# Kernel tuning notes

Hardware: AMD Instinct MI355X
Metric: run time of the kernel (lower is better)

## Reference

```python
import jax, jax.numpy as jnp
import numpy as np

HIDDEN = 1024
NUM_HEADS = 16
HEAD_DIM = HIDDEN // NUM_HEADS
SCALE = HEAD_DIM ** -0.5
BATCH = 32
T_CACHED = 2047


def setup_inputs() -> dict:
    key = jax.random.key(0)
    ks = jax.random.split(key, 8)
    hidden_states = jax.random.normal(ks[0], (BATCH, 1, HIDDEN), dtype=jnp.float32)
    key_cache = jax.random.normal(ks[1], (BATCH, NUM_HEADS, T_CACHED, HEAD_DIM), dtype=jnp.float32)
    value_cache = jax.random.normal(ks[2], (BATCH, NUM_HEADS, T_CACHED, HEAD_DIM), dtype=jnp.float32)
    block_tables = jax.random.randint(ks[3], (BATCH, 128), 0, 1024, dtype=jnp.int64 if jax.config.jax_enable_x64 else jnp.int32)
    # valid lengths in [1, T_cached+1]
    seq_lens = jax.random.randint(ks[4], (BATCH,), 1, T_CACHED + 2, dtype=jnp.int32)
    W_attn = jax.random.normal(ks[5], (HIDDEN, 3 * HIDDEN), dtype=jnp.float32) * (HIDDEN ** -0.5)
    b_attn = jnp.zeros((3 * HIDDEN,), dtype=jnp.float32)
    W_proj = jax.random.normal(ks[6], (HIDDEN, HIDDEN), dtype=jnp.float32) * (HIDDEN ** -0.5)
    b_proj = jnp.zeros((HIDDEN,), dtype=jnp.float32)
    return {
        "hidden_states": hidden_states,
        "key_cache": key_cache,
        "value_cache": value_cache,
        "block_tables": block_tables,
        "seq_lens": seq_lens,
        "max_seq_len": T_CACHED + 1,
        "W_attn": W_attn,
        "b_attn": b_attn,
        "W_proj": W_proj,
        "b_proj": b_proj,
    }


def reference(hidden_states, key_cache, value_cache, block_tables, seq_lens,
              max_seq_len, W_attn, b_attn, W_proj, b_proj):
    B, S, H = hidden_states.shape  # S == 1 (single-query decode)
    hs = hidden_states.reshape(B, H)
    qkv = hs @ W_attn + b_attn                      # [B, 3H]
    q, k, v = jnp.split(qkv, 3, axis=-1)
    q = q.reshape(B, NUM_HEADS, HEAD_DIM)           # [B, h, d]
    k = k.reshape(B, NUM_HEADS, 1, HEAD_DIM)
    v = v.reshape(B, NUM_HEADS, 1, HEAD_DIM)
    K = jnp.concatenate([key_cache, k], axis=2)     # [B, h, T, d]
    V = jnp.concatenate([value_cache, v], axis=2)
    T = K.shape[2]
    # single-query attention: scores [B, h, T]
    scores = jnp.einsum('bhd,bhtd->bht', q, K) * SCALE
    pos = jnp.arange(T)
    # attend to first seq_len cached tokens; the freshly appended token (pos T-1) is always visible
    valid = (pos[None, :] < seq_lens[:, None]) | (pos[None, :] == T - 1)  # [B, T]
    scores = jnp.where(valid[:, None, :], scores, jnp.float32(-1e30))
    p = jax.nn.softmax(scores, axis=-1)
    out = jnp.einsum('bht,bhtd->bhd', p, V)         # [B, h, d]
    attn_output = out.reshape(B, S, H) @ W_proj + b_proj
    return attn_output, K, V
```

## Files before the change

kernel.cpp:

```cpp
#include <hip/hip_runtime.h>
#include <math.h>

#define BATCH   32
#define NH      16
#define HD      64
#define T_ALL   2048
#define T_CACHE 2047
#define HID     1024
#define H3      3072
#define QK_SCALE 0.125f
#define NCHUNK  8
#define CHTOK   256
#define KSPLIT  8

typedef float f4 __attribute__((ext_vector_type(4)));

template<int NB>
__global__ __launch_bounds__(256) void gemv_part_kernel(
    const float* __restrict__ X, const float* __restrict__ W,
    float* __restrict__ part, int N, int Kdim)
{
    const int c  = blockIdx.x * 256 + threadIdx.x;
    const int ks = blockIdx.y;
    const int b0 = blockIdx.z * NB;
    const int kchunk = Kdim / KSPLIT;
    float acc[NB];
#pragma unroll
    for (int j = 0; j < NB; ++j) acc[j] = 0.f;
    const int k0 = ks * kchunk;
#pragma unroll 16
    for (int k = k0; k < k0 + kchunk; ++k) {
        const float w = W[(size_t)k * N + c];
#pragma unroll
        for (int j = 0; j < NB; ++j)
            acc[j] = fmaf(X[(b0 + j) * Kdim + k], w, acc[j]);
    }
#pragma unroll
    for (int j = 0; j < NB; ++j)
        part[((size_t)ks * BATCH + b0 + j) * N + c] = acc[j];
}

__global__ __launch_bounds__(256) void gemv_reduce_kernel(
    const float* __restrict__ part, const float* __restrict__ bias,
    float* __restrict__ out, int N)
{
    const int c4 = blockIdx.x * 256 + threadIdx.x;
    const int b  = blockIdx.y;
    const int N4 = N >> 2;
    f4 acc = ((const f4*)bias)[c4];
#pragma unroll
    for (int ks = 0; ks < KSPLIT; ++ks) {
        const f4 p = ((const f4*)part)[((size_t)ks * BATCH + b) * N4 + c4];
        acc.x += p.x; acc.y += p.y; acc.z += p.z; acc.w += p.w;
    }
    ((f4*)out)[(size_t)b * N4 + c4] = acc;
}

__global__ __launch_bounds__(256) void fused_copy_attn_kernel(
    const float* __restrict__ kc, const float* __restrict__ vc,
    const float* __restrict__ qkv, const int* __restrict__ seq_lens,
    float* __restrict__ Kout, float* __restrict__ Vout,
    float* __restrict__ Pm, float* __restrict__ Pl, float* __restrict__ Po)
{
    const int chunk = blockIdx.x;
    const int h     = blockIdx.y;
    const int b     = blockIdx.z;
    const int tid   = threadIdx.x;
    const int wave  = tid >> 6;
    const int lane  = tid & 63;
    const int dgrp  = lane & 15;
    const int tgrp  = lane >> 4;

    const int bh   = b * NH + h;
    const int slen = seq_lens[b];

    const f4 q4 = ((const f4*)(qkv + (size_t)b * H3 + h * HD))[dgrp];

    const int t0 = chunk * CHTOK + wave * 64;
    const int tl = t0 + tgrp;
    const int nat  = min(16, max(0, (slen - t0 + 3) >> 2));
    const bool tail = (t0 + 63 >= T_CACHE);

    const f4* kbase = (const f4*)(kc + (size_t)bh * T_CACHE * HD) + (size_t)tl * 16 + dgrp;
    const f4* vbase = (const f4*)(vc + (size_t)bh * T_CACHE * HD) + (size_t)tl * 16 + dgrp;
    f4* Kb = (f4*)(Kout + (size_t)bh * T_ALL * HD) + (size_t)tl * 16 + dgrp;
    f4* Vb = (f4*)(Vout + (size_t)bh * T_ALL * HD) + (size_t)tl * 16 + dgrp;

    float s[16];

    if (!tail) {
#pragma unroll
        for (int i = 0; i < 16; ++i) {
            const f4 kv = __builtin_nontemporal_load(kbase + i * 64);
            __builtin_nontemporal_store(kv, Kb + i * 64);
            if (i < nat) {
                float ss = kv.x * q4.x + kv.y * q4.y + kv.z * q4.z + kv.w * q4.w;
                ss += __shfl_xor(ss, 1);
                ss += __shfl_xor(ss, 2);
                ss += __shfl_xor(ss, 4);
                ss += __shfl_xor(ss, 8);
                s[i] = (tl + i * 4 < slen) ? ss * QK_SCALE : -1e30f;
            }
        }
    } else {
#pragma unroll
        for (int i = 0; i < 16; ++i) {
            const int t = tl + i * 4;
            f4 kv = (f4){0.f, 0.f, 0.f, 0.f};
            if (t < T_CACHE) {
                kv = __builtin_nontemporal_load(kbase + i * 64);
                __builtin_nontemporal_store(kv, Kb + i * 64);
            }
            if (i < nat) {
                float ss = kv.x * q4.x + kv.y * q4.y + kv.z * q4.z + kv.w * q4.w;
                ss += __shfl_xor(ss, 1);
                ss += __shfl_xor(ss, 2);
                ss += __shfl_xor(ss, 4);
                ss += __shfl_xor(ss, 8);
                s[i] = (t < slen && t < T_CACHE) ? ss * QK_SCALE : -1e30f;
            }
        }
    }

    float m = -1e30f;
#pragma unroll
    for (int i = 0; i < 16; ++i)
        if (i < nat) m = fmaxf(m, s[i]);
    m = fmaxf(m, __shfl_xor(m, 16));
    m = fmaxf(m, __shfl_xor(m, 32));

    float l = 0.f;
#pragma unroll
    for (int i = 0; i < 16; ++i)
        if (i < nat) {
            const float p = __expf(s[i] - m);
            s[i] = p;
            l += p;
        }

    f4 o = {0.f, 0.f, 0.f, 0.f};
    if (!tail) {
#pragma unroll
        for (int i = 0; i < 16; ++i) {
            const f4 vv = __builtin_nontemporal_load(vbase + i * 64);
            __builtin_nontemporal_store(vv, Vb + i * 64);
            if (i < nat) {
                o.x = fmaf(s[i], vv.x, o.x);
                o.y = fmaf(s[i], vv.y, o.y);
                o.z = fmaf(s[i], vv.z, o.z);
                o.w = fmaf(s[i], vv.w, o.w);
            }
        }
    } else {
#pragma unroll
        for (int i = 0; i < 16; ++i) {
            const int t = tl + i * 4;
            f4 vv = (f4){0.f, 0.f, 0.f, 0.f};
            if (t < T_CACHE) {
                vv = __builtin_nontemporal_load(vbase + i * 64);
                __builtin_nontemporal_store(vv, Vb + i * 64);
            }
            if (i < nat) {
                o.x = fmaf(s[i], vv.x, o.x);
                o.y = fmaf(s[i], vv.y, o.y);
                o.z = fmaf(s[i], vv.z, o.z);
                o.w = fmaf(s[i], vv.w, o.w);
            }
        }
    }

    l += __shfl_xor(l, 16); l += __shfl_xor(l, 32);
    o.x += __shfl_xor(o.x, 16); o.x += __shfl_xor(o.x, 32);
    o.y += __shfl_xor(o.y, 16); o.y += __shfl_xor(o.y, 32);
    o.z += __shfl_xor(o.z, 16); o.z += __shfl_xor(o.z, 32);
    o.w += __shfl_xor(o.w, 16); o.w += __shfl_xor(o.w, 32);

    __shared__ float sm[4], sl[4];
    __shared__ f4 so4[4][16];
    if (lane == 0) { sm[wave] = m; sl[wave] = l; }
    if (lane < 16) so4[wave][dgrp] = o;
    __syncthreads();

    if (tid < HD) {
        const int d = tid;
        const float m0 = sm[0], m1 = sm[1], m2 = sm[2], m3 = sm[3];
        const float mc = fmaxf(fmaxf(m0, m1), fmaxf(m2, m3));
        const float e0 = __expf(m0 - mc), e1 = __expf(m1 - mc);
        const float e2 = __expf(m2 - mc), e3 = __expf(m3 - mc);
        const float lc = sl[0]*e0 + sl[1]*e1 + sl[2]*e2 + sl[3]*e3;
        const float* so = (const float*)so4;
        const float oc = so[0*HD + d]*e0 + so[1*HD + d]*e1
                       + so[2*HD + d]*e2 + so[3*HD + d]*e3;
        const int pb = bh * NCHUNK + chunk;
        Po[(size_t)pb * HD + d] = oc;
        if (d == 0) { Pm[pb] = mc; Pl[pb] = lc; }
    }
}

__global__ __launch_bounds__(64) void combine_kernel(
    const float* __restrict__ qkv,
    const float* __restrict__ Pm, const float* __restrict__ Pl,
    const float* __restrict__ Po,
    float* __restrict__ attn, float* __restrict__ Kout, float* __restrict__ Vout)
{
    const int bh = blockIdx.x;
    const int b = bh >> 4, h = bh & 15;
    const int d = threadIdx.x;

    const float* qb = qkv + (size_t)b * H3;
    const float qd = qb[h * HD + d];
    const float kn = qb[HID  + h * HD + d];
    const float vn = qb[2*HID + h * HD + d];

    Kout[((size_t)bh * T_ALL + (T_ALL - 1)) * HD + d] = kn;
    Vout[((size_t)bh * T_ALL + (T_ALL - 1)) * HD + d] = vn;

    float s = qd * kn;
    s += __shfl_xor(s, 1);
    s += __shfl_xor(s, 2);
    s += __shfl_xor(s, 4);
    s += __shfl_xor(s, 8);
    s += __shfl_xor(s, 16);
    s += __shfl_xor(s, 32);
    s *= QK_SCALE;

    float mg = s;
#pragma unroll
    for (int c = 0; c < NCHUNK; ++c)
        mg = fmaxf(mg, Pm[bh * NCHUNK + c]);

    float L   = __expf(s - mg);
    float acc = L * vn;
#pragma unroll
    for (int c = 0; c < NCHUNK; ++c) {
        const float e = __expf(Pm[bh * NCHUNK + c] - mg);
        acc += Po[(size_t)(bh * NCHUNK + c) * HD + d] * e;
        L   += Pl[bh * NCHUNK + c] * e;
    }
    attn[(size_t)b * HID + h * HD + d] = acc / L;
}

extern "C" void kernel_launch(void* const* d_in, const int* in_sizes, int n_in,
                              void* d_out, int out_size, void* d_ws, size_t ws_size,
                              hipStream_t stream)
{
    const float* hs       = (const float*)d_in[0];
    const float* kc       = (const float*)d_in[1];
    const float* vc       = (const float*)d_in[2];
    const int*   seq_lens = (const int*)d_in[4];
    const float* W_attn   = (const float*)d_in[6];
    const float* b_attn   = (const float*)d_in[7];
    const float* W_proj   = (const float*)d_in[8];
    const float* b_proj   = (const float*)d_in[9];

    float* out_attn = (float*)d_out;
    float* Kout = out_attn + (size_t)BATCH * HID;
    float* Vout = Kout + (size_t)BATCH * NH * T_ALL * HD;

    float* w = (float*)d_ws;
    float* w_qkv_part  = w;
    float* w_qkv       = w_qkv_part + (size_t)KSPLIT * BATCH * H3;
    float* w_Pm        = w_qkv + (size_t)BATCH * H3;
    float* w_Pl        = w_Pm + BATCH * NH * NCHUNK;
    float* w_Po        = w_Pl + BATCH * NH * NCHUNK;
    float* w_attnvec   = w_Po + (size_t)BATCH * NH * NCHUNK * HD;
    float* w_proj_part = w_attnvec + (size_t)BATCH * HID;

    gemv_part_kernel<16><<<dim3(H3 / 256, KSPLIT, 2), 256, 0, stream>>>(
        hs, W_attn, w_qkv_part, H3, HID);
    gemv_reduce_kernel<<<dim3(H3 / 4 / 256, BATCH), 256, 0, stream>>>(
        w_qkv_part, b_attn, w_qkv, H3);

    fused_copy_attn_kernel<<<dim3(NCHUNK, NH, BATCH), 256, 0, stream>>>(
        kc, vc, w_qkv, seq_lens, Kout, Vout, w_Pm, w_Pl, w_Po);

    combine_kernel<<<dim3(BATCH * NH), 64, 0, stream>>>(
        w_qkv, w_Pm, w_Pl, w_Po, w_attnvec, Kout, Vout);

    gemv_part_kernel<8><<<dim3(HID / 256, KSPLIT, 4), 256, 0, stream>>>(
        w_attnvec, W_proj, w_proj_part, HID, HID);
    gemv_reduce_kernel<<<dim3(HID / 4 / 256, BATCH), 256, 0, stream>>>(
        w_proj_part, b_proj, out_attn, HID);
}
```

Before: 271.7 us.

## Issue K and V loads together up front with smaller per-block token chunks

```diff
diff --git a/kernel.cpp b/kernel.cpp
--- a/kernel.cpp
+++ b/kernel.cpp
@@ -9,8 +9,9 @@
 #define HID     1024
 #define H3      3072
 #define QK_SCALE 0.125f
-#define NCHUNK  8
-#define CHTOK   256
+#define NCHUNK  16
+#define CHTOK   128
+#define NWIN    8
 #define KSPLIT  8
 
 typedef float f4 __attribute__((ext_vector_type(4)));
@@ -56,7 +57,7 @@
     ((f4*)out)[(size_t)b * N4 + c4] = acc;
 }
 
-__global__ __launch_bounds__(256) void fused_copy_attn_kernel(
+__global__ __launch_bounds__(256, 4) void fused_copy_attn_kernel(
     const float* __restrict__ kc, const float* __restrict__ vc,
     const float* __restrict__ qkv, const int* __restrict__ seq_lens,
     float* __restrict__ Kout, float* __restrict__ Vout,
@@ -76,24 +77,32 @@
 
     const f4 q4 = ((const f4*)(qkv + (size_t)b * H3 + h * HD))[dgrp];
 
-    const int t0 = chunk * CHTOK + wave * 64;
+    const int t0 = chunk * CHTOK + wave * (NWIN * 4);
     const int tl = t0 + tgrp;
-    const int nat  = min(16, max(0, (slen - t0 + 3) >> 2));
-    const bool tail = (t0 + 63 >= T_CACHE);
+    const int nat  = min(NWIN, max(0, (slen - t0 + 3) >> 2));
+    const bool tail = (t0 + NWIN * 4 - 1 >= T_CACHE);
 
     const f4* kbase = (const f4*)(kc + (size_t)bh * T_CACHE * HD) + (size_t)tl * 16 + dgrp;
     const f4* vbase = (const f4*)(vc + (size_t)bh * T_CACHE * HD) + (size_t)tl * 16 + dgrp;
     f4* Kb = (f4*)(Kout + (size_t)bh * T_ALL * HD) + (size_t)tl * 16 + dgrp;
     f4* Vb = (f4*)(Vout + (size_t)bh * T_ALL * HD) + (size_t)tl * 16 + dgrp;
 
-    float s[16];
+    f4 kreg[NWIN], vreg[NWIN];
+    float s[NWIN];
 
     if (!tail) {
 #pragma unroll
-        for (int i = 0; i < 16; ++i) {
-            const f4 kv = __builtin_nontemporal_load(kbase + i * 64);
-            __builtin_nontemporal_store(kv, Kb + i * 64);
-            if (i < nat) {
+        for (int i = 0; i < NWIN; ++i)
+            kreg[i] = __builtin_nontemporal_load(kbase + i * 64);
+#pragma unroll
+        for (int i = 0; i < NWIN; ++i)
+            vreg[i] = __builtin_nontemporal_load(vbase + i * 64);
+
+#pragma unroll
+        for (int i = 0; i < NWIN; ++i) {
+            __builtin_nontemporal_store(kreg[i], Kb + i * 64);
+            if (i < nat) {
+                const f4 kv = kreg[i];
                 float ss = kv.x * q4.x + kv.y * q4.y + kv.z * q4.z + kv.w * q4.w;
                 ss += __shfl_xor(ss, 1);
                 ss += __shfl_xor(ss, 2);
@@ -104,14 +113,22 @@
         }
     } else {
 #pragma unroll
-        for (int i = 0; i < 16; ++i) {
+        for (int i = 0; i < NWIN; ++i) {
             const int t = tl + i * 4;
-            f4 kv = (f4){0.f, 0.f, 0.f, 0.f};
+            kreg[i] = (f4){0.f, 0.f, 0.f, 0.f};
+            vreg[i] = (f4){0.f, 0.f, 0.f, 0.f};
             if (t < T_CACHE) {
-                kv = __builtin_nontemporal_load(kbase + i * 64);
-                __builtin_nontemporal_store(kv, Kb + i * 64);
-            }
-            if (i < nat) {
+                kreg[i] = __builtin_nontemporal_load(kbase + i * 64);
+                vreg[i] = __builtin_nontemporal_load(vbase + i * 64);
+            }
+        }
+#pragma unroll
+        for (int i = 0; i < NWIN; ++i) {
+            const int t = tl + i * 4;
+            if (t < T_CACHE)
+                __builtin_nontemporal_store(kreg[i], Kb + i * 64);
+            if (i < nat) {
+                const f4 kv = kreg[i];
                 float ss = kv.x * q4.x + kv.y * q4.y + kv.z * q4.z + kv.w * q4.w;
                 ss += __shfl_xor(ss, 1);
                 ss += __shfl_xor(ss, 2);
@@ -124,14 +141,14 @@
 
     float m = -1e30f;
 #pragma unroll
-    for (int i = 0; i < 16; ++i)
+    for (int i = 0; i < NWIN; ++i)
         if (i < nat) m = fmaxf(m, s[i]);
     m = fmaxf(m, __shfl_xor(m, 16));
     m = fmaxf(m, __shfl_xor(m, 32));
 
     float l = 0.f;
 #pragma unroll
-    for (int i = 0; i < 16; ++i)
+    for (int i = 0; i < NWIN; ++i)
         if (i < nat) {
             const float p = __expf(s[i] - m);
             s[i] = p;
@@ -141,30 +158,26 @@
     f4 o = {0.f, 0.f, 0.f, 0.f};
     if (!tail) {
 #pragma unroll
-        for (int i = 0; i < 16; ++i) {
-            const f4 vv = __builtin_nontemporal_load(vbase + i * 64);
-            __builtin_nontemporal_store(vv, Vb + i * 64);
-            if (i < nat) {
-                o.x = fmaf(s[i], vv.x, o.x);
-                o.y = fmaf(s[i], vv.y, o.y);
-                o.z = fmaf(s[i], vv.z, o.z);
-                o.w = fmaf(s[i], vv.w, o.w);
+        for (int i = 0; i < NWIN; ++i) {
+            __builtin_nontemporal_store(vreg[i], Vb + i * 64);
+            if (i < nat) {
+                o.x = fmaf(s[i], vreg[i].x, o.x);
+                o.y = fmaf(s[i], vreg[i].y, o.y);
+                o.z = fmaf(s[i], vreg[i].z, o.z);
+                o.w = fmaf(s[i], vreg[i].w, o.w);
             }
         }
     } else {
 #pragma unroll
-        for (int i = 0; i < 16; ++i) {
+        for (int i = 0; i < NWIN; ++i) {
             const int t = tl + i * 4;
-            f4 vv = (f4){0.f, 0.f, 0.f, 0.f};
-            if (t < T_CACHE) {
-                vv = __builtin_nontemporal_load(vbase + i * 64);
-                __builtin_nontemporal_store(vv, Vb + i * 64);
-            }
-            if (i < nat) {
-                o.x = fmaf(s[i], vv.x, o.x);
-                o.y = fmaf(s[i], vv.y, o.y);
-                o.z = fmaf(s[i], vv.z, o.z);
-                o.w = fmaf(s[i], vv.w, o.w);
+            if (t < T_CACHE)
+                __builtin_nontemporal_store(vreg[i], Vb + i * 64);
+            if (i < nat) {
+                o.x = fmaf(s[i], vreg[i].x, o.x);
+                o.y = fmaf(s[i], vreg[i].y, o.y);
+                o.z = fmaf(s[i], vreg[i].z, o.z);
+                o.w = fmaf(s[i], vreg[i].w, o.w);
             }
         }
     }
```

Result: faster. 251.3 us (-7.5%).
